# Kernel optimization log

Measured on AMD Instinct MI355X. Metric: run time of the kernel, lower is better.

## Reference

```python
import jax, jax.numpy as jnp
import numpy as np

B, Q, K, D_TO, D_FROM, H = 16, 2048, 2048, 768, 768, 768

def setup_inputs() -> dict:
    key = jax.random.key(0)
    ks = jax.random.split(key, 8)
    s = 0.02
    return {
        "x_to": jax.random.normal(ks[0], (B, Q, D_TO), jnp.float32),
        "x_from": jax.random.normal(ks[1], (B, K, D_FROM), jnp.float32),
        "Wq": jax.random.normal(ks[2], (D_TO, H), jnp.float32) * s,
        "bq": jnp.zeros((H,), jnp.float32),
        "Wk": jax.random.normal(ks[3], (D_FROM, H), jnp.float32) * s,
        "bk": jnp.zeros((H,), jnp.float32),
        "Wv": jax.random.normal(ks[4], (D_FROM, H), jnp.float32) * s,
        "bv": jnp.zeros((H,), jnp.float32),
    }

def reference(x_to, x_from, Wq, bq, Wk, bk, Wv, bv):
    q = x_to @ Wq + bq          # [b,q,h]
    k = x_from @ Wk + bk        # [b,k,h]
    v = x_from @ Wv + bv        # [b,k,h]
    scores = jnp.einsum('bqd,bkd->bqk', q, k) / jnp.sqrt(jnp.float32(H))
    attn = jax.nn.softmax(scores, axis=-1)
    return jnp.einsum('bqk,bkd->bqd', attn, v)
```

## Files before the change

### kernel.cpp

```cpp
#include <hip/hip_runtime.h>

typedef unsigned short u16;
typedef __attribute__((ext_vector_type(8))) short s16x8;
typedef __attribute__((ext_vector_type(4))) float f32x4;

__device__ __forceinline__ u16 f2bf(float f) {
  unsigned u = __builtin_bit_cast(unsigned, f);
  return (u16)((u + 0x7fffu + ((u >> 16) & 1u)) >> 16);
}
__device__ __forceinline__ float bf2f(u16 h) {
  return __builtin_bit_cast(float, (unsigned)h << 16);
}

#define GLOAD16(gp, lp) __builtin_amdgcn_global_load_lds( \
    (__attribute__((address_space(1))) void*)(gp),        \
    (__attribute__((address_space(3))) void*)(lp), 16, 0, 0)

#define STG(p, ldx, off) do { \
    GLOAD16(p, ldst + (off)); \
    GLOAD16(p + 64 * (ldx), ldst + (off) + 8192); \
    p += 128; } while (0)

#define LD8(off) (*(const s16x8*)(ldsb + (off)))

#define MFMA2(mi, n) \
    acc[mi][n] = __builtin_amdgcn_mfma_f32_16x16x32_bf16(af[((mi)&3)*2],   bf[(n)*2],   acc[mi][n], 0,0,0); \
    acc[mi][n] = __builtin_amdgcn_mfma_f32_16x16x32_bf16(af[((mi)&3)*2+1], bf[(n)*2+1], acc[mi][n], 0,0,0);

#define PH_MID() __builtin_amdgcn_s_barrier(); \
    asm volatile("s_waitcnt lgkmcnt(0)" ::: "memory"); \
    __builtin_amdgcn_s_setprio(1)
#define PH_END() __builtin_amdgcn_s_setprio(0)

#define KTILE(BOFF, OOFF, SA1, SB2, VMW) do { \
  af[0]=LD8((BOFF)+aoff0);      af[1]=LD8((BOFF)+aoff1); \
  af[2]=LD8((BOFF)+aoff0+2048); af[3]=LD8((BOFF)+aoff1+2048); \
  af[4]=LD8((BOFF)+aoff0+4096); af[5]=LD8((BOFF)+aoff1+4096); \
  af[6]=LD8((BOFF)+aoff0+6144); af[7]=LD8((BOFF)+aoff1+6144); \
  bf[0]=LD8((BOFF)+boff0);      bf[1]=LD8((BOFF)+boff1); \
  bf[2]=LD8((BOFF)+boff0+2048); bf[3]=LD8((BOFF)+boff1+2048); \
  if (SA1) STG(pA1, ldab, (OOFF) + 16384); \
  asm volatile("s_waitcnt lgkmcnt(8)" ::: "memory"); \
  PH_MID(); \
  MFMA2(0,0) MFMA2(1,0) MFMA2(2,0) MFMA2(3,0) \
  MFMA2(0,1) MFMA2(1,1) MFMA2(2,1) MFMA2(3,1) \
  PH_END(); __builtin_amdgcn_s_barrier(); \
  bf[4]=LD8((BOFF)+boff0+4096); bf[5]=LD8((BOFF)+boff1+4096); \
  bf[6]=LD8((BOFF)+boff0+6144); bf[7]=LD8((BOFF)+boff1+6144); \
  PH_MID(); \
  MFMA2(0,2) MFMA2(1,2) MFMA2(2,2) MFMA2(3,2) \
  MFMA2(0,3) MFMA2(1,3) MFMA2(2,3) MFMA2(3,3) \
  PH_END(); __builtin_amdgcn_s_barrier(); \
  af[0]=LD8((BOFF)+aoff0+8192);  af[1]=LD8((BOFF)+aoff1+8192); \
  af[2]=LD8((BOFF)+aoff0+10240); af[3]=LD8((BOFF)+aoff1+10240); \
  af[4]=LD8((BOFF)+aoff0+12288); af[5]=LD8((BOFF)+aoff1+12288); \
  af[6]=LD8((BOFF)+aoff0+14336); af[7]=LD8((BOFF)+aoff1+14336); \
  if (SB2) STG(pB0, ldbb, (BOFF) + 32768); \
  PH_MID(); \
  MFMA2(4,0) MFMA2(5,0) MFMA2(6,0) MFMA2(7,0) \
  MFMA2(4,1) MFMA2(5,1) MFMA2(6,1) MFMA2(7,1) \
  PH_END(); __builtin_amdgcn_s_barrier(); \
  if (SB2) { STG(pB1, ldbb, (BOFF) + 49152); STG(pA0, ldab, (BOFF)); } \
  PH_MID(); \
  MFMA2(4,2) MFMA2(5,2) MFMA2(6,2) MFMA2(7,2) \
  MFMA2(4,3) MFMA2(5,3) MFMA2(6,3) MFMA2(7,3) \
  PH_END(); \
  VMW; \
  __builtin_amdgcn_s_barrier(); \
} while (0)

template<bool OUT_F32>
__global__ __launch_bounds__(512, 2) void gemm256(
    const u16* __restrict__ A, int lda, long sA,
    const u16* __restrict__ Bt, int ldb, long sB,
    void* __restrict__ Cv, int ldc, long sC,
    const float* __restrict__ bias, long biasStride, int biasMode,
    float scale, int K)
{
  __shared__ __align__(128) char ldsb[131072];
  const int tid = threadIdx.x;
  const int w = tid >> 6, l = tid & 63;
  const int wm = w >> 2, wn = w & 3;
  const int q = l >> 4, fr = l & 15;

  int bx, by;
  { int gx = gridDim.x; int nwg = gx * (int)gridDim.y;
    int id = blockIdx.y * gx + blockIdx.x;
    int qq = nwg >> 3, r = nwg & 7, xc = id & 7, ix = id >> 3;
    int swz = (xc < r ? xc * (qq + 1) : r * (qq + 1) + (xc - r) * qq) + ix;
    bx = swz % gx; by = swz / gx; }
  const long brow = (long)bx * 256, bcol = (long)by * 256;
  const int z = blockIdx.z;
  A += (long)z * sA; Bt += (long)z * sB;
  if (biasMode) bias += (long)z * biasStride;

  const long ldab = (long)lda * 2, ldbb = (long)ldb * 2;
  const int rih = w * 8 + (l >> 3);
  const int sl  = ((l & 7) ^ (l >> 3)) * 16;
  const char* pA0 = (const char*)A  + (brow + rih) * ldab + sl;
  const char* pA1 = pA0 + 128 * ldab;
  const char* pB0 = (const char*)Bt + (bcol + rih) * ldbb + sl;
  const char* pB1 = pB0 + 128 * ldbb;
  char* ldst = ldsb + w * 1024;

  const int sw = fr & 7;
  const int arow_o = (wm * 128 + fr) * 128;
  const int brow_o = (wn * 64 + fr) * 128 + 32768;
  const int aoff0 = arow_o + ((q)     ^ sw) * 16;
  const int aoff1 = arow_o + ((4 + q) ^ sw) * 16;
  const int boff0 = brow_o + ((q)     ^ sw) * 16;
  const int boff1 = brow_o + ((4 + q) ^ sw) * 16;

  f32x4 acc[8][4];
  #pragma unroll
  for (int i = 0; i < 8; ++i)
    #pragma unroll
    for (int j = 0; j < 4; ++j) acc[i][j] = (f32x4){0.f, 0.f, 0.f, 0.f};
  s16x8 af[8], bf[8];

  STG(pA0, ldab, 0);
  STG(pA1, ldab, 16384);
  STG(pB0, ldbb, 32768);
  STG(pB1, ldbb, 49152);
  asm volatile("s_waitcnt vmcnt(4)" ::: "memory");
  STG(pB0, ldbb, 65536 + 32768);
  STG(pB1, ldbb, 65536 + 49152);
  STG(pA0, ldab, 65536);
  asm volatile("s_waitcnt vmcnt(6)" ::: "memory");
  __builtin_amdgcn_s_barrier();

  const int half_iters = (K >> 7) - 1;
  for (int it = 0; it < half_iters; ++it) {
    KTILE(0,     65536, 1, 1, asm volatile("s_waitcnt vmcnt(6)" ::: "memory"));
    KTILE(65536, 0,     1, 1, asm volatile("s_waitcnt vmcnt(6)" ::: "memory"));
  }
  KTILE(0,     65536, 1, 0, asm volatile("s_waitcnt vmcnt(0)" ::: "memory"));
  KTILE(65536, 0,     0, 0, ((void)0));

  const long row0 = brow + wm * 128 + q * 4;
  const long col0 = bcol + wn * 64 + fr;
  #pragma unroll
  for (int mi = 0; mi < 8; ++mi) {
    #pragma unroll
    for (int n = 0; n < 4; ++n) {
      #pragma unroll
      for (int rr = 0; rr < 4; ++rr) {
        long row = row0 + mi * 16 + rr;
        long col = col0 + n * 16;
        float v = acc[mi][n][rr] * scale;
        if (biasMode == 1) v += bias[col];
        else if (biasMode == 2) v += bias[row];
        if constexpr (OUT_F32)
          ((float*)Cv)[(long)z * sC + row * (long)ldc + col] = v;
        else
          ((u16*)Cv)[(long)z * sC + row * (long)ldc + col] = f2bf(v);
      }
    }
  }
}

__global__ __launch_bounds__(256) void cvt_x2(const float4* __restrict__ xt,
                                              const float4* __restrict__ xf,
                                              u16* __restrict__ out, long NX) {
  const float4* src = blockIdx.y ? xf : xt;
  u16* dst = out + (long)blockIdx.y * NX;
  long i = (long)blockIdx.x * 256 + threadIdx.x;
  float4 v = src[i];
  uint2 o;
  o.x = (unsigned)f2bf(v.x) | ((unsigned)f2bf(v.y) << 16);
  o.y = (unsigned)f2bf(v.z) | ((unsigned)f2bf(v.w) << 16);
  *(uint2*)(dst + i * 4) = o;
}

__global__ __launch_bounds__(256) void cvt_w3(const float* __restrict__ W0,
                                              const float* __restrict__ W1,
                                              const float* __restrict__ W2,
                                              u16* __restrict__ WT) {
  const float* W = blockIdx.y == 0 ? W0 : (blockIdx.y == 1 ? W1 : W2);
  u16* dst = WT + (long)blockIdx.y * 589824;
  int idx = blockIdx.x * 256 + threadIdx.x;
  int h = idx / 768, d = idx - h * 768;
  dst[idx] = f2bf(W[d * 768 + h]);
}

__global__ __launch_bounds__(256) void pack_bias(const float* __restrict__ bq,
                                                 const float* __restrict__ bk,
                                                 float* __restrict__ out) {
  int i = blockIdx.x * 256 + threadIdx.x;
  out[i] = i < 768 ? bq[i] : bk[i - 768];
}

__global__ __launch_bounds__(256) void softmax_rows(u16* __restrict__ S) {
  const int t = threadIdx.x;
  const int wave = t >> 6, lane = t & 63;
  u16* row = S + (long)blockIdx.x * 2048;
  s16x8 v = *(const s16x8*)(row + t * 8);
  float f[8];
  #pragma unroll
  for (int j = 0; j < 8; ++j) f[j] = bf2f((u16)v[j]);
  float mx = f[0];
  #pragma unroll
  for (int j = 1; j < 8; ++j) mx = fmaxf(mx, f[j]);
  #pragma unroll
  for (int off = 32; off > 0; off >>= 1) mx = fmaxf(mx, __shfl_xor(mx, off, 64));
  __shared__ float smax[4];
  __shared__ float ssum[4];
  if (lane == 0) smax[wave] = mx;
  __syncthreads();
  mx = fmaxf(fmaxf(smax[0], smax[1]), fmaxf(smax[2], smax[3]));
  float s = 0.f;
  #pragma unroll
  for (int j = 0; j < 8; ++j) { f[j] = __expf(f[j] - mx); s += f[j]; }
  #pragma unroll
  for (int off = 32; off > 0; off >>= 1) s += __shfl_xor(s, off, 64);
  if (lane == 0) ssum[wave] = s;
  __syncthreads();
  s = (ssum[0] + ssum[1]) + (ssum[2] + ssum[3]);
  float inv = 1.f / s;
  s16x8 o;
  #pragma unroll
  for (int j = 0; j < 8; ++j) o[j] = (short)f2bf(f[j] * inv);
  *(s16x8*)(row + t * 8) = o;
}

extern "C" void kernel_launch(void* const* d_in, const int* in_sizes, int n_in,
                              void* d_out, int out_size, void* d_ws, size_t ws_size,
                              hipStream_t stream) {
  const float* x_to   = (const float*)d_in[0];
  const float* x_from = (const float*)d_in[1];
  const float* Wq = (const float*)d_in[2];
  const float* bq = (const float*)d_in[3];
  const float* Wk = (const float*)d_in[4];
  const float* bk = (const float*)d_in[5];
  const float* Wv = (const float*)d_in[6];
  const float* bv = (const float*)d_in[7];

  const long NX = 16L * 2048 * 768;
  const long NW = 768L * 768;

  u16* Qb  = (u16*)d_ws;
  u16* Kb  = Qb + NX;
  u16* Vt  = Kb + NX;
  u16* reg2 = Vt + NX;
  u16* Sb  = reg2;
  u16* xtb = reg2;
  u16* xfb = xtb + NX;
  u16* WqT = xfb + NX;
  float* bqk = (float*)(WqT + 3 * NW);

  cvt_x2<<<dim3(24576, 2), 256, 0, stream>>>((const float4*)x_to,
                                             (const float4*)x_from, xtb, NX);
  cvt_w3<<<dim3(2304, 3), 256, 0, stream>>>(Wq, Wk, Wv, WqT);
  pack_bias<<<6, 256, 0, stream>>>(bq, bk, bqk);

  dim3 blk(512);
  gemm256<false><<<dim3(128, 3, 2), blk, 0, stream>>>(
      xtb, 768, NX, WqT, 768, NW, Qb, 768, NX, bqk, 768, 1, 1.f, 768);
  gemm256<false><<<dim3(3, 128, 1), blk, 0, stream>>>(
      WqT + 2 * NW, 768, 0, xfb, 768, 0, Vt, 32768, 0, bv, 0, 2, 1.f, 768);
  gemm256<false><<<dim3(8, 8, 16), blk, 0, stream>>>(
      Qb, 768, 2048L * 768, Kb, 768, 2048L * 768,
      Sb, 2048, 2048L * 2048, nullptr, 0, 0, 0.036084391824351615f, 768);
  softmax_rows<<<32768, 256, 0, stream>>>(Sb);
  gemm256<true><<<dim3(8, 3, 16), blk, 0, stream>>>(
      Sb, 2048, 2048L * 2048, Vt, 32768, 2048,
      (float*)d_out, 768, 2048L * 768, nullptr, 0, 0, 1.f, 2048);
}
```

Before: 763.0 us.

## Pad per-batch V-transpose layout and reorder MFMA issue to break accumulator chains

The transposed V projection is now written per batch with a padded leading dimension (2176, falling back to 2048 if workspace is short) instead of one 32768-wide row. The PV GEMM reads V through this padded per-batch stride. The padding is meant to avoid LDS and channel conflicts caused by power-of-two strides. Separately, the MFMA issue order in each phase is interleaved so consecutive MFMAs write different accumulators, reducing back-to-back dependency stalls.

```diff
diff --git a/kernel.cpp b/kernel.cpp
--- a/kernel.cpp
+++ b/kernel.cpp
@@ -23,9 +23,26 @@
 
 #define LD8(off) (*(const s16x8*)(ldsb + (off)))
 
-#define MFMA2(mi, n) \
-    acc[mi][n] = __builtin_amdgcn_mfma_f32_16x16x32_bf16(af[((mi)&3)*2],   bf[(n)*2],   acc[mi][n], 0,0,0); \
-    acc[mi][n] = __builtin_amdgcn_mfma_f32_16x16x32_bf16(af[((mi)&3)*2+1], bf[(n)*2+1], acc[mi][n], 0,0,0);
+#define MF(a, b, c) __builtin_amdgcn_mfma_f32_16x16x32_bf16(a, b, c, 0, 0, 0)
+
+#define PH_MFMA(MB, NB) do { \
+  acc[(MB)+0][(NB)]   = MF(af[0], bf[(NB)*2],   acc[(MB)+0][(NB)]); \
+  acc[(MB)+1][(NB)]   = MF(af[2], bf[(NB)*2],   acc[(MB)+1][(NB)]); \
+  acc[(MB)+2][(NB)]   = MF(af[4], bf[(NB)*2],   acc[(MB)+2][(NB)]); \
+  acc[(MB)+3][(NB)]   = MF(af[6], bf[(NB)*2],   acc[(MB)+3][(NB)]); \
+  acc[(MB)+0][(NB)+1] = MF(af[0], bf[(NB)*2+2], acc[(MB)+0][(NB)+1]); \
+  acc[(MB)+1][(NB)+1] = MF(af[2], bf[(NB)*2+2], acc[(MB)+1][(NB)+1]); \
+  acc[(MB)+2][(NB)+1] = MF(af[4], bf[(NB)*2+2], acc[(MB)+2][(NB)+1]); \
+  acc[(MB)+3][(NB)+1] = MF(af[6], bf[(NB)*2+2], acc[(MB)+3][(NB)+1]); \
+  acc[(MB)+0][(NB)]   = MF(af[1], bf[(NB)*2+1], acc[(MB)+0][(NB)]); \
+  acc[(MB)+1][(NB)]   = MF(af[3], bf[(NB)*2+1], acc[(MB)+1][(NB)]); \
+  acc[(MB)+2][(NB)]   = MF(af[5], bf[(NB)*2+1], acc[(MB)+2][(NB)]); \
+  acc[(MB)+3][(NB)]   = MF(af[7], bf[(NB)*2+1], acc[(MB)+3][(NB)]); \
+  acc[(MB)+0][(NB)+1] = MF(af[1], bf[(NB)*2+3], acc[(MB)+0][(NB)+1]); \
+  acc[(MB)+1][(NB)+1] = MF(af[3], bf[(NB)*2+3], acc[(MB)+1][(NB)+1]); \
+  acc[(MB)+2][(NB)+1] = MF(af[5], bf[(NB)*2+3], acc[(MB)+2][(NB)+1]); \
+  acc[(MB)+3][(NB)+1] = MF(af[7], bf[(NB)*2+3], acc[(MB)+3][(NB)+1]); \
+} while (0)
 
 #define PH_MID() __builtin_amdgcn_s_barrier(); \
     asm volatile("s_waitcnt lgkmcnt(0)" ::: "memory"); \
@@ -42,14 +59,12 @@
   if (SA1) STG(pA1, ldab, (OOFF) + 16384); \
   asm volatile("s_waitcnt lgkmcnt(8)" ::: "memory"); \
   PH_MID(); \
-  MFMA2(0,0) MFMA2(1,0) MFMA2(2,0) MFMA2(3,0) \
-  MFMA2(0,1) MFMA2(1,1) MFMA2(2,1) MFMA2(3,1) \
+  PH_MFMA(0, 0); \
   PH_END(); __builtin_amdgcn_s_barrier(); \
   bf[4]=LD8((BOFF)+boff0+4096); bf[5]=LD8((BOFF)+boff1+4096); \
   bf[6]=LD8((BOFF)+boff0+6144); bf[7]=LD8((BOFF)+boff1+6144); \
   PH_MID(); \
-  MFMA2(0,2) MFMA2(1,2) MFMA2(2,2) MFMA2(3,2) \
-  MFMA2(0,3) MFMA2(1,3) MFMA2(2,3) MFMA2(3,3) \
+  PH_MFMA(0, 2); \
   PH_END(); __builtin_amdgcn_s_barrier(); \
   af[0]=LD8((BOFF)+aoff0+8192);  af[1]=LD8((BOFF)+aoff1+8192); \
   af[2]=LD8((BOFF)+aoff0+10240); af[3]=LD8((BOFF)+aoff1+10240); \
@@ -57,13 +72,11 @@
   af[6]=LD8((BOFF)+aoff0+14336); af[7]=LD8((BOFF)+aoff1+14336); \
   if (SB2) STG(pB0, ldbb, (BOFF) + 32768); \
   PH_MID(); \
-  MFMA2(4,0) MFMA2(5,0) MFMA2(6,0) MFMA2(7,0) \
-  MFMA2(4,1) MFMA2(5,1) MFMA2(6,1) MFMA2(7,1) \
+  PH_MFMA(4, 0); \
   PH_END(); __builtin_amdgcn_s_barrier(); \
   if (SB2) { STG(pB1, ldbb, (BOFF) + 49152); STG(pA0, ldab, (BOFF)); } \
   PH_MID(); \
-  MFMA2(4,2) MFMA2(5,2) MFMA2(6,2) MFMA2(7,2) \
-  MFMA2(4,3) MFMA2(5,3) MFMA2(6,3) MFMA2(7,3) \
+  PH_MFMA(4, 2); \
   PH_END(); \
   VMW; \
   __builtin_amdgcn_s_barrier(); \
@@ -238,10 +251,17 @@
   const long NX = 16L * 2048 * 768;
   const long NW = 768L * 768;
 
+  long ldv = 2176;
+  {
+    long need = (2 * NX + 16L * 768 * ldv + 16L * 2048 * 2048) * 2;
+    if (need > (long)ws_size) ldv = 2048;
+  }
+  const long VT = 16L * 768 * ldv;
+
   u16* Qb  = (u16*)d_ws;
   u16* Kb  = Qb + NX;
   u16* Vt  = Kb + NX;
-  u16* reg2 = Vt + NX;
+  u16* reg2 = Vt + VT;
   u16* Sb  = reg2;
   u16* xtb = reg2;
   u16* xfb = xtb + NX;
@@ -256,13 +276,14 @@
   dim3 blk(512);
   gemm256<false><<<dim3(128, 3, 2), blk, 0, stream>>>(
       xtb, 768, NX, WqT, 768, NW, Qb, 768, NX, bqk, 768, 1, 1.f, 768);
-  gemm256<false><<<dim3(3, 128, 1), blk, 0, stream>>>(
-      WqT + 2 * NW, 768, 0, xfb, 768, 0, Vt, 32768, 0, bv, 0, 2, 1.f, 768);
+  gemm256<false><<<dim3(3, 8, 16), blk, 0, stream>>>(
+      WqT + 2 * NW, 768, 0, xfb, 768, 2048L * 768,
+      Vt, (int)ldv, 768L * ldv, bv, 0, 2, 1.f, 768);
   gemm256<false><<<dim3(8, 8, 16), blk, 0, stream>>>(
       Qb, 768, 2048L * 768, Kb, 768, 2048L * 768,
       Sb, 2048, 2048L * 2048, nullptr, 0, 0, 0.036084391824351615f, 768);
   softmax_rows<<<32768, 256, 0, stream>>>(Sb);
   gemm256<true><<<dim3(8, 3, 16), blk, 0, stream>>>(
-      Sb, 2048, 2048L * 2048, Vt, 32768, 2048,
+      Sb, 2048, 2048L * 2048, Vt, (int)ldv, 768L * ldv,
       (float*)d_out, 768, 2048L * 768, nullptr, 0, 0, 1.f, 2048);
 }
```

After: 761.8 us. About the same (-0.2%).
